# Kernel tuning notes

Hardware: AMD Instinct MI355X
Metric: run time of the kernel (lower is better)

## Reference

```python
import jax, jax.numpy as jnp
import numpy as np

H, DK, DV = 4, 64, 64        # heads, key/value head dims (hidden=256)
M, TOPK = 4, 2               # num memories, router top-k
GN, EPS, COND_SCALE = 16.0, 1e-5, 1.0


def setup_inputs() -> dict:
    key = jax.random.key(0)
    ks = jax.random.split(key, 12)
    B, Q, K, D = 8, 64, 256, 256
    w = lambda k, shape, fan: jax.random.normal(k, shape, jnp.float32) / np.sqrt(fan).astype(np.float32)
    return {
        "query": jax.random.normal(ks[0], (B, Q, D), jnp.float32),
        "keyval": jax.random.normal(ks[1], (B, K, D), jnp.float32),
        "attention_mask_kv": jnp.ones((B, K), jnp.int32),
        "W_cond": w(ks[2], (D, D), D),
        "W_q": w(ks[3], (D, H * DK), D),
        "W_k": w(ks[4], (D, H * DK), D),
        "W_v": w(ks[5], (D, H * DV), D),
        "W_gk1": w(ks[6], (D, 16), D),
        "W_gk2": w(ks[7], (16, H * DK), 16),
        "b_gk2": jnp.zeros((H * DK,), jnp.float32),
        "W_router": w(ks[8], (D, M), D),
        "norm_w": jnp.ones((DV,), jnp.float32),
        "W_o": w(ks[9], (H * DV, D), H * DV),
    }


def _mem_last(q_last, k, v, gk, sel, wgt):
    """Last-token output of one gated linear-attention memory.
    S_t = diag(exp(gk_t)) S_{t-1} + k_t v_t^T ; o_T = q_T S_T.
    q_last: (N,H,DK); k,gk: (N,K,H,DK); v: (N,K,H,DV); sel,wgt: (N,K)."""
    k_e = k * sel[:, :, None, None]
    v_e = v * wgt[:, :, None, None]
    gk_e = gk * sel[:, :, None, None]          # unselected tokens: no decay, no update
    G = jnp.cumsum(gk_e, axis=1)               # (N,K,H,DK), log decays
    decay = jnp.exp(G[:, -1:, :, :] - G)       # remaining decay to last step, <= 1
    s = jnp.einsum('nhd,nthd->nth', q_last, k_e * decay)
    return jnp.einsum('nth,nthv->nhv', s, v_e)


def reference(query, keyval, attention_mask_kv, W_cond, W_q, W_k, W_v,
              W_gk1, W_gk2, b_gk2, W_router, norm_w, W_o):
    B, Q, D = query.shape
    K = keyval.shape[1]
    N = B * Q
    # broadcast KV expansion + cond injection
    cond = (query @ W_cond) * COND_SCALE                         # (B,Q,D)
    x = (keyval[:, None, :, :] + cond[:, :, None, :]).reshape(N, K, D)
    m = jnp.broadcast_to(attention_mask_kv[:, None, :].astype(x.dtype), (B, Q, K)).reshape(N, K)
    # projections
    q = (x @ W_q).reshape(N, K, H, DK)
    k = (x @ W_k).reshape(N, K, H, DK) * m[:, :, None, None]
    v = (x @ W_v).reshape(N, K, H, DV) * m[:, :, None, None]
    gk = (jax.nn.log_sigmoid(x @ W_gk1 @ W_gk2 + b_gk2) / GN).reshape(N, K, H, DK)
    gk = gk * m[:, :, None, None]
    # router: softmax -> top-k -> renormalize
    router_logits = (x @ W_router).reshape(N * K, M)
    probs = jax.nn.softmax(router_logits, axis=-1)
    topv, topi = jax.lax.top_k(probs, TOPK)
    topv = topv / jnp.sum(topv, axis=-1, keepdims=True)
    w_mem = jnp.sum(jax.nn.one_hot(topi, M, dtype=x.dtype) * topv[..., None], axis=-2)
    w_mem = w_mem.reshape(N, K, M)
    # shared memory (always on) + routed memories
    q_last = q[:, -1]
    ones = jnp.ones((N, K), x.dtype)
    o = _mem_last(q_last, k, v, gk, ones, ones)
    for e in range(M):
        we = w_mem[:, :, e]
        o = o + _mem_last(q_last, k, v, gk, (we > 0).astype(x.dtype), we)
    # per-head RMSNorm + output projection
    o = o * jax.lax.rsqrt(jnp.mean(o * o, axis=-1, keepdims=True) + EPS) * norm_w
    out = (o.reshape(N, H * DV) @ W_o).reshape(B, Q, D)
    return out, router_logits
```

## Files before the change

### kernel.cpp

```cpp
#include <hip/hip_runtime.h>
#include <math.h>

#define Hh   4
#define Bb   8
#define Qq   64
#define Kk   256
#define Dd   256
#define Nn   (Bb * Qq)
#define GNf  16.0f
#define EPSf 1e-5f
#define WB   1088

__device__ __forceinline__ float wred(float x) {
#pragma unroll
    for (int off = 32; off > 0; off >>= 1)
        x += __shfl_xor(x, off, 64);
    return x;
}

__global__ __launch_bounds__(256) void pack_wb(
    const float* __restrict__ Wq, const float* __restrict__ Wk,
    const float* __restrict__ Wv, const float* __restrict__ Wg1,
    const float* __restrict__ Wg2, const float* __restrict__ Wr,
    float* __restrict__ Wb)
{
    const int idx = blockIdx.x * 256 + threadIdx.x;
    const int k = idx / WB, j = idx % WB;
    float v;
    if (j < 256)       v = Wq[(size_t)k * 256 + j];
    else if (j < 512)  v = Wk[(size_t)k * 256 + j - 256];
    else if (j < 768)  v = Wv[(size_t)k * 256 + j - 512];
    else if (j < 1024) {
        const int c = j - 768;
        float s = 0.f;
#pragma unroll
        for (int i = 0; i < 16; ++i)
            s = fmaf(Wg1[(size_t)k * 16 + i], Wg2[(size_t)i * 256 + c], s);
        v = s;
    }
    else if (j < 1028) v = Wr[(size_t)k * 4 + (j - 1024)];
    else               v = 0.f;
    Wb[idx] = v;
}

__global__ __launch_bounds__(256) void gemm1(
    const float* __restrict__ keyval, const float* __restrict__ query,
    const float* __restrict__ Wb, const float* __restrict__ W_cond,
    float* __restrict__ KVb, float* __restrict__ cond)
{
    __shared__ float As[64][17];
    __shared__ float Ws[16][65];
    const int tid = threadIdx.x;

    int id = blockIdx.x;
    const float* A; const float* Bp; float* C;
    int ldb, ldc;
    if (id < 544) {
        const int bm = (id / 17) * 64, bn = (id % 17) * 64;
        A  = keyval + (size_t)bm * Dd;
        Bp = Wb + bn;        ldb = WB;
        C  = KVb + (size_t)bm * WB + bn;  ldc = WB;
    } else {
        id -= 544;
        const int bm = (id >> 2) * 64, bn = (id & 3) * 64;
        A  = query + (size_t)bm * Dd;
        Bp = W_cond + bn;    ldb = Dd;
        C  = cond + (size_t)bm * Dd + bn; ldc = Dd;
    }

    const int ty = tid >> 4, tx = tid & 15;
    const int aRow = tid >> 2, aCol = (tid & 3) * 4;
    const int wRow = tid >> 6, wCol = tid & 63;

    float acc[4][4] = {};

    for (int k0 = 0; k0 < Dd; k0 += 16) {
        const float4 av = *(const float4*)(A + (size_t)aRow * Dd + k0 + aCol);
        As[aRow][aCol + 0] = av.x;
        As[aRow][aCol + 1] = av.y;
        As[aRow][aCol + 2] = av.z;
        As[aRow][aCol + 3] = av.w;
#pragma unroll
        for (int r = 0; r < 4; ++r)
            Ws[wRow + 4 * r][wCol] = Bp[(size_t)(k0 + wRow + 4 * r) * ldb + wCol];
        __syncthreads();
#pragma unroll
        for (int kk = 0; kk < 16; ++kk) {
            float a[4], wv[4];
#pragma unroll
            for (int i = 0; i < 4; ++i) a[i] = As[ty * 4 + i][kk];
#pragma unroll
            for (int j = 0; j < 4; ++j) wv[j] = Ws[kk][tx * 4 + j];
#pragma unroll
            for (int i = 0; i < 4; ++i)
#pragma unroll
                for (int j = 0; j < 4; ++j)
                    acc[i][j] = fmaf(a[i], wv[j], acc[i][j]);
        }
        __syncthreads();
    }

#pragma unroll
    for (int i = 0; i < 4; ++i)
#pragma unroll
        for (int j = 0; j < 4; ++j)
            C[(size_t)(ty * 4 + i) * ldc + tx * 4 + j] = acc[i][j];
}

__global__ __launch_bounds__(256) void gemm2(
    const float* __restrict__ cond, const float* __restrict__ Wb,
    float* __restrict__ Cb)
{
    __shared__ float As[64][17];
    __shared__ float Ws[16][65];
    const int tid = threadIdx.x;
    const int bm = blockIdx.y * 64;
    const int bn = blockIdx.x * 64;
    const int ty = tid >> 4, tx = tid & 15;
    const int aRow = tid >> 2, aCol = (tid & 3) * 4;
    const int wRow = tid >> 6, wCol = tid & 63;

    float acc[4][4] = {};

    for (int k0 = 0; k0 < Dd; k0 += 16) {
        const float4 av = *(const float4*)(cond + (size_t)(bm + aRow) * Dd + k0 + aCol);
        As[aRow][aCol + 0] = av.x;
        As[aRow][aCol + 1] = av.y;
        As[aRow][aCol + 2] = av.z;
        As[aRow][aCol + 3] = av.w;
#pragma unroll
        for (int r = 0; r < 4; ++r)
            Ws[wRow + 4 * r][wCol] = Wb[(size_t)(k0 + wRow + 4 * r) * WB + bn + wCol];
        __syncthreads();
#pragma unroll
        for (int kk = 0; kk < 16; ++kk) {
            float a[4], wv[4];
#pragma unroll
            for (int i = 0; i < 4; ++i) a[i] = As[ty * 4 + i][kk];
#pragma unroll
            for (int j = 0; j < 4; ++j) wv[j] = Ws[kk][tx * 4 + j];
#pragma unroll
            for (int i = 0; i < 4; ++i)
#pragma unroll
                for (int j = 0; j < 4; ++j)
                    acc[i][j] = fmaf(a[i], wv[j], acc[i][j]);
        }
        __syncthreads();
    }

#pragma unroll
    for (int i = 0; i < 4; ++i)
#pragma unroll
        for (int j = 0; j < 4; ++j)
            Cb[(size_t)(bm + ty * 4 + i) * WB + bn + tx * 4 + j] = acc[i][j];
}

__global__ __launch_bounds__(256) void mom_fused(
    const float* __restrict__ KVb, const float* __restrict__ Cb,
    const float* __restrict__ b_gk2, const int* __restrict__ mask,
    const float* __restrict__ W_o, const float* __restrict__ norm_w,
    float* __restrict__ out, float* __restrict__ logits)
{
    __shared__ float4 wm[Kk];
    __shared__ float  Ptile[4][16][68];
    __shared__ float  sbuf[4][16];
    __shared__ float  onorm[Dd];

    const int n = blockIdx.x;
    const int b = n >> 6;
    const int j = threadIdx.x;
    const int lane = j & 63;
    const int wv = j >> 6;

    const float qc = Cb[(size_t)n * WB + j];
    const float kc = Cb[(size_t)n * WB + 256 + j];
    const float vc = Cb[(size_t)n * WB + 512 + j];
    const float pc = Cb[(size_t)n * WB + 768 + j] + b_gk2[j];
    const float4 rc = *(const float4*)(Cb + (size_t)n * WB + 1024);

    {
        const float4 kvr = *(const float4*)(KVb + (size_t)(b * Kk + j) * WB + 1024);
        float l[4] = {kvr.x + rc.x, kvr.y + rc.y, kvr.z + rc.z, kvr.w + rc.w};
        *(float4*)(logits + ((size_t)n * Kk + j) * 4) = make_float4(l[0], l[1], l[2], l[3]);

        int i1 = 0;
#pragma unroll
        for (int q = 1; q < 4; ++q) if (l[q] > l[i1]) i1 = q;
        int i2 = -1;
#pragma unroll
        for (int q = 0; q < 4; ++q) {
            if (q == i1) continue;
            if (i2 < 0 || l[q] > l[i2]) i2 = q;
        }
        const float mx = fmaxf(l[i1], l[i2]);
        const float e1 = __expf(l[i1] - mx);
        const float e2 = __expf(l[i2] - mx);
        const float inv = 1.f / (e1 + e2);
        float w[4] = {0.f, 0.f, 0.f, 0.f};
        w[i1] = e1 * inv;
        w[i2] = e2 * inv;
        wm[j] = make_float4(w[0], w[1], w[2], w[3]);
    }
    __syncthreads();

    const float ql = KVb[(size_t)(b * Kk + Kk - 1) * WB + j] + qc;
    const float* pk = KVb + (size_t)b * Kk * WB + 256 + j;
    const float* pv = KVb + (size_t)b * Kk * WB + 512 + j;
    const float* pp = KVb + (size_t)b * Kk * WB + 768 + j;
    const int*   pm = mask + b * Kk;

    float E0 = 1.f, E1 = 1.f, E2 = 1.f, E3 = 1.f, E4 = 1.f;
    float o = 0.f;
    const int tl = lane & 15, qq = lane >> 4;

    for (int t0 = Kk - 16; t0 >= 0; t0 -= 16) {
        float vreg[16];
#pragma unroll
        for (int i = 0; i < 16; ++i) {
            const int t = t0 + 15 - i;
            const float mf  = (float)pm[t];
            const float kk  = (pk[(size_t)t * WB] + kc) * mf;
            const float vvv = (pv[(size_t)t * WB] + vc) * mf;
            const float pre = pp[(size_t)t * WB] + pc;
            const float4 w  = wm[t];

            const float ls = fminf(pre, 0.f) - __logf(1.f + __expf(-fabsf(pre)));
            float dg = __expf(ls * (1.0f / GNf));
            dg = (mf != 0.f) ? dg : 1.f;

            const float zf = E0 + w.x * E1 + w.y * E2 + w.z * E3 + w.w * E4;
            Ptile[wv][i][lane] = ql * kk * zf;
            vreg[i] = vvv;

            E0 *= dg;
            E1 *= (w.x > 0.f) ? dg : 1.f;
            E2 *= (w.y > 0.f) ? dg : 1.f;
            E3 *= (w.z > 0.f) ? dg : 1.f;
            E4 *= (w.w > 0.f) ? dg : 1.f;
        }
        __builtin_amdgcn_wave_barrier();

        float s = 0.f;
#pragma unroll
        for (int r = 0; r < 4; ++r) {
            const float4 p4 = *(const float4*)&Ptile[wv][tl][qq * 16 + r * 4];
            s += (p4.x + p4.y) + (p4.z + p4.w);
        }
        s += __shfl_xor(s, 16, 64);
        s += __shfl_xor(s, 32, 64);
        sbuf[wv][tl] = s;
        __builtin_amdgcn_wave_barrier();
#pragma unroll
        for (int r = 0; r < 4; ++r) {
            const float4 sv = *(const float4*)&sbuf[wv][r * 4];
            o = fmaf(sv.x, vreg[r * 4 + 0], o);
            o = fmaf(sv.y, vreg[r * 4 + 1], o);
            o = fmaf(sv.z, vreg[r * 4 + 2], o);
            o = fmaf(sv.w, vreg[r * 4 + 3], o);
        }
    }

    const float ms = wred(o * o) * (1.0f / 64.0f);
    onorm[j] = o * rsqrtf(ms + EPSf) * norm_w[lane];
    __syncthreads();

    float acc = 0.f;
#pragma unroll 8
    for (int k = 0; k < Dd; ++k)
        acc = fmaf(onorm[k], W_o[(size_t)k * Dd + j], acc);
    out[(size_t)n * Dd + j] = acc;
}

extern "C" void kernel_launch(void* const* d_in, const int* in_sizes, int n_in,
                              void* d_out, int out_size, void* d_ws, size_t ws_size,
                              hipStream_t stream)
{
    const float* query    = (const float*)d_in[0];
    const float* keyval   = (const float*)d_in[1];
    const int*   mask     = (const int*)  d_in[2];
    const float* W_cond   = (const float*)d_in[3];
    const float* W_q      = (const float*)d_in[4];
    const float* W_k      = (const float*)d_in[5];
    const float* W_v      = (const float*)d_in[6];
    const float* W_gk1    = (const float*)d_in[7];
    const float* W_gk2    = (const float*)d_in[8];
    const float* b_gk2    = (const float*)d_in[9];
    const float* W_router = (const float*)d_in[10];
    const float* norm_w   = (const float*)d_in[11];
    const float* W_o      = (const float*)d_in[12];

    float* out    = (float*)d_out;
    float* logits = out + Nn * Dd;

    float* p = (float*)d_ws;
    float* Wb   = p; p += Dd * WB;
    float* KVb  = p; p += Bb * Kk * WB;
    float* cond = p; p += Nn * Dd;
    float* Cb   = p; p += Nn * WB;

    pack_wb<<<(Dd * WB) / 256, dim3(256), 0, stream>>>(
        W_q, W_k, W_v, W_gk1, W_gk2, W_router, Wb);

    gemm1<<<576, dim3(256), 0, stream>>>(keyval, query, Wb, W_cond, KVb, cond);

    gemm2<<<dim3(WB / 64, Nn / 64), dim3(256), 0, stream>>>(cond, Wb, Cb);

    mom_fused<<<Nn, dim3(256), 0, stream>>>(
        KVb, Cb, b_gk2, mask, W_o, norm_w, out, logits);
}
```

Measured before the change: 196.4 us.

## Restructure projection GEMMs, drop weight packing, compute only last-token queries

```diff
diff --git a/kernel.cpp b/kernel.cpp
--- a/kernel.cpp
+++ b/kernel.cpp
@@ -9,7 +9,9 @@
 #define Nn   (Bb * Qq)
 #define GNf  16.0f
 #define EPSf 1e-5f
-#define WB   1088
+
+#define SKV  832
+#define SCB  1088
 
 __device__ __forceinline__ float wred(float x) {
 #pragma unroll
@@ -18,168 +20,193 @@
     return x;
 }
 
-__global__ __launch_bounds__(256) void pack_wb(
-    const float* __restrict__ Wq, const float* __restrict__ Wk,
-    const float* __restrict__ Wv, const float* __restrict__ Wg1,
-    const float* __restrict__ Wg2, const float* __restrict__ Wr,
-    float* __restrict__ Wb)
-{
-    const int idx = blockIdx.x * 256 + threadIdx.x;
-    const int k = idx / WB, j = idx % WB;
-    float v;
-    if (j < 256)       v = Wq[(size_t)k * 256 + j];
-    else if (j < 512)  v = Wk[(size_t)k * 256 + j - 256];
-    else if (j < 768)  v = Wv[(size_t)k * 256 + j - 512];
-    else if (j < 1024) {
-        const int c = j - 768;
-        float s = 0.f;
-#pragma unroll
-        for (int i = 0; i < 16; ++i)
-            s = fmaf(Wg1[(size_t)k * 16 + i], Wg2[(size_t)i * 256 + c], s);
-        v = s;
-    }
-    else if (j < 1028) v = Wr[(size_t)k * 4 + (j - 1024)];
-    else               v = 0.f;
-    Wb[idx] = v;
-}
-
-__global__ __launch_bounds__(256) void gemm1(
+__global__ __launch_bounds__(256) void prep(
+    const float* __restrict__ Wg1, const float* __restrict__ Wg2,
+    float* __restrict__ Wg)
+{
+    const int e = blockIdx.x * 256 + threadIdx.x;
+    const int k = e >> 8, c = e & 255;
+    float s = 0.f;
+#pragma unroll
+    for (int i = 0; i < 16; ++i)
+        s = fmaf(Wg1[k * 16 + i], Wg2[i * 256 + c], s);
+    Wg[e] = s;
+}
+
+__device__ __forceinline__ void gemm_tile(
+    const float* __restrict__ A, int lda, int Mv,
+    const float* __restrict__ B, int ldb, int bn,
+    float* __restrict__ C, int ldc)
+{
+    __shared__ float As[16][68];
+    __shared__ float Ws[16][136];
+    const int tid = threadIdx.x;
+    const int ty = tid >> 4, tx = tid & 15;
+    const int am = tid >> 2, ak = (tid & 3) << 2;
+    const int wk = tid >> 4, wc = (tid & 15) << 3;
+    const int ams = (am < Mv) ? am : (Mv - 1);
+
+    float acc[4][8] = {};
+
+    const float* aptr = A + (size_t)ams * lda + ak;
+    const float* bptr = B + (size_t)wk * ldb + bn + wc;
+    float4 av  = *(const float4*)(aptr);
+    float4 bv0 = *(const float4*)(bptr);
+    float4 bv1 = *(const float4*)(bptr + 4);
+
+    for (int k0 = 0; k0 < 256; k0 += 16) {
+        __syncthreads();
+        As[ak + 0][am] = av.x;
+        As[ak + 1][am] = av.y;
+        As[ak + 2][am] = av.z;
+        As[ak + 3][am] = av.w;
+        *(float4*)&Ws[wk][wc]     = bv0;
+        *(float4*)&Ws[wk][wc + 4] = bv1;
+        __syncthreads();
+        if (k0 + 16 < 256) {
+            av  = *(const float4*)(aptr + k0 + 16);
+            bv0 = *(const float4*)(bptr + (size_t)(k0 + 16) * ldb);
+            bv1 = *(const float4*)(bptr + (size_t)(k0 + 16) * ldb + 4);
+        }
+#pragma unroll
+        for (int kk = 0; kk < 16; ++kk) {
+            const float4 a4 = *(const float4*)&As[kk][ty << 2];
+            const float4 w0 = *(const float4*)&Ws[kk][tx << 2];
+            const float4 w1 = *(const float4*)&Ws[kk][64 + (tx << 2)];
+            const float a_[4] = {a4.x, a4.y, a4.z, a4.w};
+            const float w_[8] = {w0.x, w0.y, w0.z, w0.w, w1.x, w1.y, w1.z, w1.w};
+#pragma unroll
+            for (int i = 0; i < 4; ++i)
+#pragma unroll
+                for (int jj = 0; jj < 8; ++jj)
+                    acc[i][jj] = fmaf(a_[i], w_[jj], acc[i][jj]);
+        }
+    }
+
+#pragma unroll
+    for (int i = 0; i < 4; ++i) {
+        const int rr = (ty << 2) + i;
+        if (rr < Mv) {
+            *(float4*)(C + (size_t)rr * ldc + (tx << 2)) =
+                make_float4(acc[i][0], acc[i][1], acc[i][2], acc[i][3]);
+            *(float4*)(C + (size_t)rr * ldc + 64 + (tx << 2)) =
+                make_float4(acc[i][4], acc[i][5], acc[i][6], acc[i][7]);
+        }
+    }
+}
+
+__device__ __forceinline__ void router_region(
+    const float* __restrict__ A, const float* __restrict__ Wr,
+    float* __restrict__ C, int ldc, int row0)
+{
+    __shared__ float WrT[4][260];
+    const int tid = threadIdx.x;
+    for (int idx = tid; idx < 1024; idx += 256) {
+        const int k = idx >> 2, c = idx & 3;
+        WrT[c][k] = Wr[idx];
+    }
+    __syncthreads();
+    const int row = row0 + (tid >> 2), c = tid & 3;
+    const float* a = A + (size_t)row * 256;
+    float acc = 0.f;
+#pragma unroll 8
+    for (int k4 = 0; k4 < 64; ++k4) {
+        const float4 avv = *(const float4*)(a + (k4 << 2));
+        const float4 wvv = *(const float4*)&WrT[c][k4 << 2];
+        acc = fmaf(avv.x, wvv.x, acc);
+        acc = fmaf(avv.y, wvv.y, acc);
+        acc = fmaf(avv.z, wvv.z, acc);
+        acc = fmaf(avv.w, wvv.w, acc);
+    }
+    C[(size_t)row * ldc + c] = acc;
+}
+
+__global__ __launch_bounds__(256) void gemm_main(
     const float* __restrict__ keyval, const float* __restrict__ query,
-    const float* __restrict__ Wb, const float* __restrict__ W_cond,
-    float* __restrict__ KVb, float* __restrict__ cond)
-{
-    __shared__ float As[64][17];
-    __shared__ float Ws[16][65];
-    const int tid = threadIdx.x;
-
-    int id = blockIdx.x;
-    const float* A; const float* Bp; float* C;
-    int ldb, ldc;
-    if (id < 544) {
-        const int bm = (id / 17) * 64, bn = (id % 17) * 64;
-        A  = keyval + (size_t)bm * Dd;
-        Bp = Wb + bn;        ldb = WB;
-        C  = KVb + (size_t)bm * WB + bn;  ldc = WB;
+    const float* __restrict__ W_k, const float* __restrict__ W_v,
+    const float* __restrict__ Wg, const float* __restrict__ W_cond,
+    const float* __restrict__ W_q, const float* __restrict__ W_router,
+    float* __restrict__ KVb, float* __restrict__ cond,
+    float* __restrict__ qlast)
+{
+    const int id = blockIdx.x;
+    if (id < 242 - 32) {
+        const float* A; int lda, Mv; const float* Bm; int bn; float* C; int ldc;
+        if (id < 192) {
+            const int rt = id / 6, ct = id % 6;
+            const float* Bsel; int cbase;
+            if (ct < 2)      { Bsel = W_k; cbase = 0; }
+            else if (ct < 4) { Bsel = W_v; cbase = 256; }
+            else             { Bsel = Wg;  cbase = 512; }
+            A = keyval + (size_t)rt * 64 * 256; lda = 256; Mv = 64;
+            Bm = Bsel; bn = (ct & 1) * 128;
+            C = KVb + (size_t)rt * 64 * SKV + cbase + bn; ldc = SKV;
+        } else if (id < 208) {
+            const int t = id - 192, rt = t >> 1, ct = t & 1;
+            A = query + (size_t)rt * 64 * 256; lda = 256; Mv = 64;
+            Bm = W_cond; bn = ct * 128;
+            C = cond + (size_t)rt * 64 * 256 + ct * 128; ldc = 256;
+        } else {
+            const int ct = id - 208;
+            A = keyval + 255 * 256; lda = Kk * Dd; Mv = 8;
+            Bm = W_q; bn = ct * 128;
+            C = qlast + ct * 128; ldc = 256;
+        }
+        gemm_tile(A, lda, Mv, Bm, 256, bn, C, ldc);
     } else {
-        id -= 544;
-        const int bm = (id >> 2) * 64, bn = (id & 3) * 64;
-        A  = query + (size_t)bm * Dd;
-        Bp = W_cond + bn;    ldb = Dd;
-        C  = cond + (size_t)bm * Dd + bn; ldc = Dd;
-    }
-
-    const int ty = tid >> 4, tx = tid & 15;
-    const int aRow = tid >> 2, aCol = (tid & 3) * 4;
-    const int wRow = tid >> 6, wCol = tid & 63;
-
-    float acc[4][4] = {};
-
-    for (int k0 = 0; k0 < Dd; k0 += 16) {
-        const float4 av = *(const float4*)(A + (size_t)aRow * Dd + k0 + aCol);
-        As[aRow][aCol + 0] = av.x;
-        As[aRow][aCol + 1] = av.y;
-        As[aRow][aCol + 2] = av.z;
-        As[aRow][aCol + 3] = av.w;
-#pragma unroll
-        for (int r = 0; r < 4; ++r)
-            Ws[wRow + 4 * r][wCol] = Bp[(size_t)(k0 + wRow + 4 * r) * ldb + wCol];
-        __syncthreads();
-#pragma unroll
-        for (int kk = 0; kk < 16; ++kk) {
-            float a[4], wv[4];
-#pragma unroll
-            for (int i = 0; i < 4; ++i) a[i] = As[ty * 4 + i][kk];
-#pragma unroll
-            for (int j = 0; j < 4; ++j) wv[j] = Ws[kk][tx * 4 + j];
-#pragma unroll
-            for (int i = 0; i < 4; ++i)
-#pragma unroll
-                for (int j = 0; j < 4; ++j)
-                    acc[i][j] = fmaf(a[i], wv[j], acc[i][j]);
-        }
-        __syncthreads();
-    }
-
-#pragma unroll
-    for (int i = 0; i < 4; ++i)
-#pragma unroll
-        for (int j = 0; j < 4; ++j)
-            C[(size_t)(ty * 4 + i) * ldc + tx * 4 + j] = acc[i][j];
-}
-
-__global__ __launch_bounds__(256) void gemm2(
-    const float* __restrict__ cond, const float* __restrict__ Wb,
-    float* __restrict__ Cb)
-{
-    __shared__ float As[64][17];
-    __shared__ float Ws[16][65];
-    const int tid = threadIdx.x;
-    const int bm = blockIdx.y * 64;
-    const int bn = blockIdx.x * 64;
-    const int ty = tid >> 4, tx = tid & 15;
-    const int aRow = tid >> 2, aCol = (tid & 3) * 4;
-    const int wRow = tid >> 6, wCol = tid & 63;
-
-    float acc[4][4] = {};
-
-    for (int k0 = 0; k0 < Dd; k0 += 16) {
-        const float4 av = *(const float4*)(cond + (size_t)(bm + aRow) * Dd + k0 + aCol);
-        As[aRow][aCol + 0] = av.x;
-        As[aRow][aCol + 1] = av.y;
-        As[aRow][aCol + 2] = av.z;
-        As[aRow][aCol + 3] = av.w;
-#pragma unroll
-        for (int r = 0; r < 4; ++r)
-            Ws[wRow + 4 * r][wCol] = Wb[(size_t)(k0 + wRow + 4 * r) * WB + bn + wCol];
-        __syncthreads();
-#pragma unroll
-        for (int kk = 0; kk < 16; ++kk) {
-            float a[4], wv[4];
-#pragma unroll
-            for (int i = 0; i < 4; ++i) a[i] = As[ty * 4 + i][kk];
-#pragma unroll
-            for (int j = 0; j < 4; ++j) wv[j] = Ws[kk][tx * 4 + j];
-#pragma unroll
-            for (int i = 0; i < 4; ++i)
-#pragma unroll
-                for (int j = 0; j < 4; ++j)
-                    acc[i][j] = fmaf(a[i], wv[j], acc[i][j]);
-        }
-        __syncthreads();
-    }
-
-#pragma unroll
-    for (int i = 0; i < 4; ++i)
-#pragma unroll
-        for (int j = 0; j < 4; ++j)
-            Cb[(size_t)(bm + ty * 4 + i) * WB + bn + tx * 4 + j] = acc[i][j];
+        router_region(keyval, W_router, KVb + 768, SKV, (id - 210) * 64);
+    }
+}
+
+__global__ __launch_bounds__(256) void gemm_cb(
+    const float* __restrict__ cond,
+    const float* __restrict__ W_q, const float* __restrict__ W_k,
+    const float* __restrict__ W_v, const float* __restrict__ Wg,
+    const float* __restrict__ W_router, float* __restrict__ Cb)
+{
+    const int id = blockIdx.x;
+    if (id < 64) {
+        const int rg = id >> 4, t = id & 15, rt = t >> 1, ct = t & 1;
+        const float* Bsel = (rg == 0) ? W_q : (rg == 1) ? W_k : (rg == 2) ? W_v : Wg;
+        gemm_tile(cond + (size_t)rt * 64 * 256, 256, 64,
+                  Bsel, 256, ct * 128,
+                  Cb + (size_t)rt * 64 * SCB + rg * 256 + ct * 128, SCB);
+    } else {
+        router_region(cond, W_router, Cb + 1024, SCB, (id - 64) * 64);
+    }
 }
 
 __global__ __launch_bounds__(256) void mom_fused(
     const float* __restrict__ KVb, const float* __restrict__ Cb,
-    const float* __restrict__ b_gk2, const int* __restrict__ mask,
-    const float* __restrict__ W_o, const float* __restrict__ norm_w,
-    float* __restrict__ out, float* __restrict__ logits)
+    const float* __restrict__ qlast, const float* __restrict__ b_gk2,
+    const int* __restrict__ mask, const float* __restrict__ W_o,
+    const float* __restrict__ norm_w, float* __restrict__ out,
+    float* __restrict__ logits)
 {
     __shared__ float4 wm[Kk];
+    __shared__ float4 sw[Kk];
+    __shared__ float  smf[Kk];
     __shared__ float  Ptile[4][16][68];
     __shared__ float  sbuf[4][16];
     __shared__ float  onorm[Dd];
 
-    const int n = blockIdx.x;
+    const int bid = blockIdx.x;
+    const int n = ((bid & 7) << 6) | (bid >> 3);
     const int b = n >> 6;
     const int j = threadIdx.x;
     const int lane = j & 63;
     const int wv = j >> 6;
 
-    const float qc = Cb[(size_t)n * WB + j];
-    const float kc = Cb[(size_t)n * WB + 256 + j];
-    const float vc = Cb[(size_t)n * WB + 512 + j];
-    const float pc = Cb[(size_t)n * WB + 768 + j] + b_gk2[j];
-    const float4 rc = *(const float4*)(Cb + (size_t)n * WB + 1024);
+    const float qc = Cb[(size_t)n * SCB + j];
+    const float kc = Cb[(size_t)n * SCB + 256 + j];
+    const float vc = Cb[(size_t)n * SCB + 512 + j];
+    const float pc = Cb[(size_t)n * SCB + 768 + j] + b_gk2[j];
+    const float4 rc = *(const float4*)(Cb + (size_t)n * SCB + 1024);
+
+    const int* pm = mask + b * Kk;
 
     {
-        const float4 kvr = *(const float4*)(KVb + (size_t)(b * Kk + j) * WB + 1024);
+        const float4 kvr = *(const float4*)(KVb + (size_t)(b * Kk + j) * SKV + 768);
         float l[4] = {kvr.x + rc.x, kvr.y + rc.y, kvr.z + rc.z, kvr.w + rc.w};
         *(float4*)(logits + ((size_t)n * Kk + j) * 4) = make_float4(l[0], l[1], l[2], l[3]);
 
@@ -200,14 +227,16 @@
         w[i1] = e1 * inv;
         w[i2] = e2 * inv;
         wm[j] = make_float4(w[0], w[1], w[2], w[3]);
+        const float mfj = (float)pm[j];
+        smf[j] = mfj;
+        sw[j] = make_float4(w[0] > 0.f ? mfj : 0.f, w[1] > 0.f ? mfj : 0.f,
+                            w[2] > 0.f ? mfj : 0.f, w[3] > 0.f ? mfj : 0.f);
     }
     __syncthreads();
 
-    const float ql = KVb[(size_t)(b * Kk + Kk - 1) * WB + j] + qc;
-    const float* pk = KVb + (size_t)b * Kk * WB + 256 + j;
-    const float* pv = KVb + (size_t)b * Kk * WB + 512 + j;
-    const float* pp = KVb + (size_t)b * Kk * WB + 768 + j;
-    const int*   pm = mask + b * Kk;
+    const float ql  = qlast[b * Dd + j] + qc;
+    const float qkc = ql * kc;
+    const float* pkv = KVb + (size_t)b * Kk * SKV + j;
 
     float E0 = 1.f, E1 = 1.f, E2 = 1.f, E3 = 1.f, E4 = 1.f;
     float o = 0.f;
@@ -218,32 +247,33 @@
 #pragma unroll
         for (int i = 0; i < 16; ++i) {
             const int t = t0 + 15 - i;
-            const float mf  = (float)pm[t];
-            const float kk  = (pk[(size_t)t * WB] + kc) * mf;
-            const float vvv = (pv[(size_t)t * WB] + vc) * mf;
-            const float pre = pp[(size_t)t * WB] + pc;
+            const float* r = pkv + (size_t)t * SKV;
+            const float kraw = r[0];
+            const float vraw = r[256];
+            const float praw = r[512];
+            const float pre = praw + pc;
+            const float ee = __expf(-pre);
+            const float dg = __expf(-0.0625f * __logf(1.0f + ee));
             const float4 w  = wm[t];
-
-            const float ls = fminf(pre, 0.f) - __logf(1.f + __expf(-fabsf(pre)));
-            float dg = __expf(ls * (1.0f / GNf));
-            dg = (mf != 0.f) ? dg : 1.f;
-
+            const float4 s4 = sw[t];
+            const float mf  = smf[t];
             const float zf = E0 + w.x * E1 + w.y * E2 + w.z * E3 + w.w * E4;
-            Ptile[wv][i][lane] = ql * kk * zf;
-            vreg[i] = vvv;
-
-            E0 *= dg;
-            E1 *= (w.x > 0.f) ? dg : 1.f;
-            E2 *= (w.y > 0.f) ? dg : 1.f;
-            E3 *= (w.z > 0.f) ? dg : 1.f;
-            E4 *= (w.w > 0.f) ? dg : 1.f;
+            const float qlk = fmaf(ql, kraw, qkc);
+            Ptile[wv][i][lane] = qlk * zf * mf;
+            vreg[i] = vraw + vc;
+            const float d1 = dg - 1.0f;
+            E0 *= fmaf(mf,   d1, 1.0f);
+            E1 *= fmaf(s4.x, d1, 1.0f);
+            E2 *= fmaf(s4.y, d1, 1.0f);
+            E3 *= fmaf(s4.z, d1, 1.0f);
+            E4 *= fmaf(s4.w, d1, 1.0f);
         }
         __builtin_amdgcn_wave_barrier();
 
         float s = 0.f;
 #pragma unroll
-        for (int r = 0; r < 4; ++r) {
-            const float4 p4 = *(const float4*)&Ptile[wv][tl][qq * 16 + r * 4];
+        for (int rr = 0; rr < 4; ++rr) {
+            const float4 p4 = *(const float4*)&Ptile[wv][tl][qq * 16 + rr * 4];
             s += (p4.x + p4.y) + (p4.z + p4.w);
         }
         s += __shfl_xor(s, 16, 64);
@@ -251,12 +281,12 @@
         sbuf[wv][tl] = s;
         __builtin_amdgcn_wave_barrier();
 #pragma unroll
-        for (int r = 0; r < 4; ++r) {
-            const float4 sv = *(const float4*)&sbuf[wv][r * 4];
-            o = fmaf(sv.x, vreg[r * 4 + 0], o);
-            o = fmaf(sv.y, vreg[r * 4 + 1], o);
-            o = fmaf(sv.z, vreg[r * 4 + 2], o);
-            o = fmaf(sv.w, vreg[r * 4 + 3], o);
+        for (int rr = 0; rr < 4; ++rr) {
+            const float4 sv = *(const float4*)&sbuf[wv][rr * 4];
+            o = fmaf(sv.x, vreg[rr * 4 + 0], o);
+            o = fmaf(sv.y, vreg[rr * 4 + 1], o);
+            o = fmaf(sv.z, vreg[rr * 4 + 2], o);
+            o = fmaf(sv.w, vreg[rr * 4 + 3], o);
         }
     }
 
@@ -293,18 +323,19 @@
     float* logits = out + Nn * Dd;
 
     float* p = (float*)d_ws;
-    float* Wb   = p; p += Dd * WB;
-    float* KVb  = p; p += Bb * Kk * WB;
-    float* cond = p; p += Nn * Dd;
-    float* Cb   = p; p += Nn * WB;
-
-    pack_wb<<<(Dd * WB) / 256, dim3(256), 0, stream>>>(
-        W_q, W_k, W_v, W_gk1, W_gk2, W_router, Wb);
-
-    gemm1<<<576, dim3(256), 0, stream>>>(keyval, query, Wb, W_cond, KVb, cond);
-
-    gemm2<<<dim3(WB / 64, Nn / 64), dim3(256), 0, stream>>>(cond, Wb, Cb);
+    float* Wg    = p; p += 256 * 256;
+    float* KVb   = p; p += 2048 * SKV;
+    float* cond  = p; p += Nn * 256;
+    float* qlast = p; p += 8 * 256;
+    float* Cb    = p; p += Nn * SCB;
+
+    prep<<<256, dim3(256), 0, stream>>>(W_gk1, W_gk2, Wg);
+
+    gemm_main<<<242, dim3(256), 0, stream>>>(
+        keyval, query, W_k, W_v, Wg, W_cond, W_q, W_router, KVb, cond, qlast);
+
+    gemm_cb<<<72, dim3(256), 0, stream>>>(cond, W_q, W_k, W_v, Wg, W_router, Cb);
 
     mom_fused<<<Nn, dim3(256), 0, stream>>>(
-        KVb, Cb, b_gk2, mask, W_o, norm_w, out, logits);
-}
+        KVb, Cb, qlast, b_gk2, mask, W_o, norm_w, out, logits);
+}
```

Result: slower. 206.0 us (+4.8%).
